# Kernel optimization log

Hardware: AMD Instinct MI355X
Metric: run time of the kernel (lower is better)

The kernel has to match this reference:

```python
import jax, jax.numpy as jnp
import numpy as np
from jax import lax

EPS = 1e-5  # BatchNorm eps (eval mode, running stats)
HEADS = 8

# --- surrogate-gradient Heaviside (sigmoid surrogate, alpha=4) ---
@jax.custom_vjp
def spike(u):
    return (u >= 0.0).astype(u.dtype)

def _spike_fwd(u):
    return spike(u), u

def _spike_bwd(u, g):
    s = jax.nn.sigmoid(4.0 * u)
    return (g * 4.0 * s * (1.0 - s),)

spike.defvjp(_spike_fwd, _spike_bwd)

def lif(x, tau=0.5, threshold=1.0):
    """Multi-step LIF over leading time axis: v_t = tau*v_{t-1} + x_t,
    s_t = H(v_t - threshold), hard reset v_t *= (1 - s_t)."""
    def step(v, xt):
        v = tau * v + xt
        s = spike(v - threshold)
        return v * (1.0 - s), s
    _, out = lax.scan(step, jnp.zeros_like(x[0]), x)
    return out

def bn_eval(x, gamma, beta, mean, var):
    # x: (T,B,C,N); per-channel affine using running stats
    inv = gamma / jnp.sqrt(var + EPS)
    return x * inv[None, None, :, None] + (beta - mean * inv)[None, None, :, None]

def setup_inputs() -> dict:
    key = jax.random.key(0)
    ks = jax.random.split(key, 12)
    T, B, C, H, W = 4, 32, 384, 16, 16
    d = {}
    d['x'] = jax.random.normal(ks[0], (T, B, C, H, W), dtype=jnp.float32)
    # 1x1 Conv1d weights == (C_out, C_in) matrices
    sc = 1.0 / np.sqrt(C)
    d['q_w'] = jax.random.normal(ks[1], (C, C), dtype=jnp.float32) * sc
    d['q_gamma'] = jnp.ones((C,), jnp.float32)
    d['q_beta'] = jnp.zeros((C,), jnp.float32)
    d['q_mean'] = jax.random.normal(ks[2], (C,), dtype=jnp.float32) * 0.1
    d['q_var'] = jax.random.uniform(ks[3], (C,), dtype=jnp.float32) + 0.5
    d['k_w'] = jax.random.normal(ks[4], (C, C), dtype=jnp.float32) * sc
    d['k_gamma'] = jnp.ones((C,), jnp.float32)
    d['k_beta'] = jnp.zeros((C,), jnp.float32)
    d['k_mean'] = jax.random.normal(ks[5], (C,), dtype=jnp.float32) * 0.1
    d['k_var'] = jax.random.uniform(ks[6], (C,), dtype=jnp.float32) + 0.5
    d['proj_w'] = jax.random.normal(ks[7], (C, C), dtype=jnp.float32) * sc
    d['proj_b'] = jax.random.normal(ks[8], (C,), dtype=jnp.float32) * 0.01
    d['proj_gamma'] = jnp.ones((C,), jnp.float32)
    d['proj_beta'] = jnp.zeros((C,), jnp.float32)
    d['proj_mean'] = jax.random.normal(ks[9], (C,), dtype=jnp.float32) * 0.1
    d['proj_var'] = jax.random.uniform(ks[10], (C,), dtype=jnp.float32) + 0.5
    d['mem_alpha'] = jnp.float32(0.2)
    return d

def reference(x, q_w, q_gamma, q_beta, q_mean, q_var,
              k_w, k_gamma, k_beta, k_mean, k_var,
              proj_w, proj_b, proj_gamma, proj_beta, proj_mean, proj_var,
              mem_alpha):
    T, B, C, H, W = x.shape
    Hh = HEADS
    Dh = C // Hh
    N = H * W
    # proj_lif applied to raw input, then flatten spatial dims
    s = lif(x, tau=0.5, threshold=1.0).reshape(T, B, C, N)
    # q path: 1x1 conv (channel GEMM) -> BN -> LIF
    q = lif(bn_eval(jnp.einsum('tbcn,dc->tbdn', s, q_w), q_gamma, q_beta, q_mean, q_var),
            tau=0.5, threshold=1.0).reshape(T, B, Hh, Dh, N)
    # k path
    k = lif(bn_eval(jnp.einsum('tbcn,dc->tbdn', s, k_w), k_gamma, k_beta, k_mean, k_var),
            tau=0.5, threshold=1.0).reshape(T, B, Hh, Dh, N)
    # temporal decayed memory: m_0 = q_0; m_t = alpha*m_{t-1} + (1-alpha)*q_{t-1}
    def mstep(m_prev, q_prev):
        m = mem_alpha * m_prev + (1.0 - mem_alpha) * q_prev
        return m, m
    _, mems_rest = lax.scan(mstep, q[0], q[:-1])
    mems = jnp.concatenate([q[:1], mems_rest], axis=0)  # (T,B,Hh,Dh,N)
    # cat along Dh then sum == sum(mems)+sum(q)
    q_sum = jnp.sum(mems, axis=3, keepdims=True) + jnp.sum(q, axis=3, keepdims=True)
    attn = lif(q_sum, tau=0.5, threshold=0.5)  # (T,B,Hh,1,N)
    y = (attn * k).reshape(T, B, C, N)
    # proj conv (with bias) -> BN -> reshape back to (T,B,C,H,W)
    y = jnp.einsum('tbcn,dc->tbdn', y, proj_w) + proj_b[None, None, :, None]
    y = bn_eval(y, proj_gamma, proj_beta, proj_mean, proj_var)
    return y.reshape(T, B, C, H, W)
```

## Files before the change

kernel.cpp:

```cpp
#include <hip/hip_runtime.h>

#define T_ 4
#define B_ 32
#define C_ 384
#define N_ 256
#define HEADS_ 8
#define DH_ 48
#define EPS_ 1e-5f
#define NW_ (C_*C_)

typedef _Float16 f16;
typedef __attribute__((ext_vector_type(8))) _Float16 f16x8;
typedef __attribute__((ext_vector_type(16))) float f32x16;

#define PSCALE     4096.0f
#define PSCALE_INV (1.0f/4096.0f)
#define SPIKE_BYTE 0x3Cu

__device__ __forceinline__ void unpack4(unsigned int w, unsigned int& lo, unsigned int& hi) {
#if defined(__has_builtin) && __has_builtin(__builtin_amdgcn_perm)
    lo = __builtin_amdgcn_perm(w, w, 0x010C000Cu);
    hi = __builtin_amdgcn_perm(w, w, 0x030C020Cu);
#else
    lo = ((w & 0xFFu) << 8) | ((w & 0xFF00u) << 16);
    hi = ((w & 0x00FF0000u) >> 8) | (w & 0xFF000000u);
#endif
}

__global__ __launch_bounds__(256)
void prep_kernel(const float* __restrict__ x, f16* __restrict__ s,
                 const float* __restrict__ qw, const float* __restrict__ kw,
                 const float* __restrict__ pw,
                 f16* __restrict__ q2, f16* __restrict__ k2, f16* __restrict__ p2)
{
    if (blockIdx.z == 32) {
        const int base = (blockIdx.y * 4 + blockIdx.x) * 256 + threadIdx.x;
        int idx = base;
#pragma unroll 4
        for (int it = 0; it < 48; ++it) {
            {
                float w = qw[idx]; f16 a = (f16)w; f16 bb = (f16)((w - (float)a) * PSCALE);
                q2[idx] = a; q2[NW_ + idx] = bb;
            }
            {
                float w = kw[idx]; f16 a = (f16)w; f16 bb = (f16)((w - (float)a) * PSCALE);
                k2[idx] = a; k2[NW_ + idx] = bb;
            }
            {
                float w = pw[idx]; f16 a = (f16)w; f16 bb = (f16)((w - (float)a) * PSCALE);
                p2[idx] = a; p2[NW_ + idx] = bb;
            }
            idx += 3072;
        }
        return;
    }

    const int tid = threadIdx.x;
    const int ng = tid & 15;
    const int cg = tid >> 4;
    const int n4 = blockIdx.x * 64 + ng * 4;
    const int c0 = blockIdx.y * 128 + cg * 8;
    const int b  = blockIdx.z;

    float v[8][4];
#pragma unroll
    for (int i = 0; i < 8; ++i)
#pragma unroll
        for (int j = 0; j < 4; ++j) v[i][j] = 0.f;

#pragma unroll
    for (int t = 0; t < T_; ++t) {
        const float* xt = x + (((size_t)t * B_ + b) * C_) * N_;
        float4 xv[8];
#pragma unroll
        for (int i = 0; i < 8; ++i)
            xv[i] = *(const float4*)&xt[(size_t)(c0 + i) * N_ + n4];
#pragma unroll
        for (int j = 0; j < 4; ++j) {
            union { f16 h[8]; uint4 q; } u;
#pragma unroll
            for (int i = 0; i < 8; ++i) {
                float xa = (j == 0) ? xv[i].x : (j == 1) ? xv[i].y
                         : (j == 2) ? xv[i].z : xv[i].w;
                float vv = 0.5f * v[i][j] + xa;
                int sp = (vv >= 1.0f) ? 1 : 0;
                v[i][j] = sp ? 0.f : vv;
                u.h[i] = sp ? (f16)1.0f : (f16)0.0f;
            }
            f16* dst = s + (((size_t)t * B_ + b) * N_ + n4 + j) * (size_t)C_ + c0;
            *(uint4*)dst = u.q;
        }
    }
}

__global__ __launch_bounds__(256)
void qk_gemm_lif_kernel(const f16* __restrict__ Wq, const f16* __restrict__ Wk,
                        const f16* __restrict__ S,
                        const float* __restrict__ qg, const float* __restrict__ qb,
                        const float* __restrict__ qm, const float* __restrict__ qv,
                        const float* __restrict__ kg, const float* __restrict__ kb,
                        const float* __restrict__ km, const float* __restrict__ kv,
                        unsigned char* __restrict__ q_spk,
                        unsigned char* __restrict__ k_spk)
{
    __shared__ __align__(16) char smem[36864];
    f16 (*As)[72]      = reinterpret_cast<f16(*)[72]>(smem);
    f16 (*Bs)[64][72]  = reinterpret_cast<f16(*)[64][72]>(smem + 18432);

    const int tid  = threadIdx.x;
    const int lane = tid & 63;
    const int wave = tid >> 6;
    const int wm = wave & 1, wd = wave >> 1;
    const int l31 = lane & 31;
    const int lhi = lane >> 5;

    const int mb = blockIdx.x;
    const int b  = mb >> 3;
    const int n0 = (mb & 7) * 32;
    const int dp0 = blockIdx.y * 64;
    const int path = (dp0 >= C_) ? 1 : 0;
    const int d0 = dp0 - path * C_;

    const f16* W = path ? Wk : Wq;
    const float* g_  = path ? kg : qg;
    const float* be_ = path ? kb : qb;
    const float* m_  = path ? km : qm;
    const float* va_ = path ? kv : qv;
    unsigned char* spk = path ? k_spk : q_spk;

    const int dcol = d0 + wd * 32 + l31;
    const float inv = g_[dcol] / sqrtf(va_[dcol] + EPS_);
    const float add = be_[dcol] - m_[dcol] * inv;

    const int ar = tid >> 1;
    const int ah = (tid & 1) * 32;
    const int at = ar >> 5;
    const int anl = ar & 31;
    const f16* arow = S + (((size_t)at * B_ + b) * N_ + n0 + anl) * (size_t)C_;
    const int aps = 4 * anl + ((at + (anl >> 1)) & 3);

    const int bp = tid >> 7;
    const int brr = (tid >> 1) & 63;
    const int bh = (tid & 1) * 32;
    const f16* brow = W + (size_t)bp * NW_ + (size_t)(d0 + brr) * C_;

    const int abase = 4 * (l31 >> 2) + ((l31 + (l31 >> 3)) & 3);
    const f16* pa0 = &As[wm * 64 + abase][0];
    const f16* pa1 = pa0 + 32 * 72;

    f32x16 acc[2][2];
#pragma unroll
    for (int ms = 0; ms < 2; ++ms)
#pragma unroll
        for (int p = 0; p < 2; ++p)
#pragma unroll
            for (int r = 0; r < 16; ++r) acc[ms][p][r] = 0.f;

    for (int kc = 0; kc < C_; kc += 64) {
        __syncthreads();
        {
            const f16* ga = arow + kc + ah;
            *(uint4*)&As[aps][ah]      = *(const uint4*)(ga);
            *(uint4*)&As[aps][ah + 8]  = *(const uint4*)(ga + 8);
            *(uint4*)&As[aps][ah + 16] = *(const uint4*)(ga + 16);
            *(uint4*)&As[aps][ah + 24] = *(const uint4*)(ga + 24);
            const f16* gb = brow + kc + bh;
            *(uint4*)&Bs[bp][brr][bh]      = *(const uint4*)(gb);
            *(uint4*)&Bs[bp][brr][bh + 8]  = *(const uint4*)(gb + 8);
            *(uint4*)&Bs[bp][brr][bh + 16] = *(const uint4*)(gb + 16);
            *(uint4*)&Bs[bp][brr][bh + 24] = *(const uint4*)(gb + 24);
        }
        __syncthreads();
#pragma unroll
        for (int kk = 0; kk < 4; ++kk) {
            const int ko = kk * 16 + lhi * 8;
            f16x8 a0 = *(const f16x8*)(pa0 + ko);
            f16x8 a1 = *(const f16x8*)(pa1 + ko);
            f16x8 b0 = *(const f16x8*)&Bs[0][wd * 32 + l31][ko];
            f16x8 b1 = *(const f16x8*)&Bs[1][wd * 32 + l31][ko];
            acc[0][0] = __builtin_amdgcn_mfma_f32_32x32x16_f16(a0, b0, acc[0][0], 0, 0, 0);
            acc[1][0] = __builtin_amdgcn_mfma_f32_32x32x16_f16(a1, b0, acc[1][0], 0, 0, 0);
            acc[0][1] = __builtin_amdgcn_mfma_f32_32x32x16_f16(a0, b1, acc[0][1], 0, 0, 0);
            acc[1][1] = __builtin_amdgcn_mfma_f32_32x32x16_f16(a1, b1, acc[1][1], 0, 0, 0);
        }
    }

#pragma unroll
    for (int ms = 0; ms < 2; ++ms)
#pragma unroll
    for (int g = 0; g < 4; ++g) {
        const int n = n0 + wm * 16 + ms * 8 + 2 * g + lhi;
        float v = 0.f;
#pragma unroll
        for (int t = 0; t < 4; ++t) {
            const int r = g * 4 + t;
            float val = (acc[ms][0][r] + acc[ms][1][r] * PSCALE_INV) * inv + add;
            float vv = 0.5f * v + val;
            int sp = (vv >= 1.0f) ? 1 : 0;
            v = sp ? 0.f : vv;
            spk[(((size_t)t * B_ + b) * N_ + n) * C_ + dcol] =
                sp ? (unsigned char)SPIKE_BYTE : (unsigned char)0;
        }
    }
}

__global__ __launch_bounds__(256)
void head_attn_kernel(const unsigned char* __restrict__ q_spk,
                      const float* __restrict__ alpha_p,
                      unsigned char* __restrict__ attn)
{
    int i = blockIdx.x * 256 + threadIdx.x;
    int n = i & (N_ - 1);
    int h = (i >> 8) & (HEADS_ - 1);
    int b = i >> 11;
    const float alpha = alpha_p[0];
    const int stride = B_ * HEADS_ * N_;
    float M = 0.f, v = 0.f, Sprev = 0.f;
#pragma unroll
    for (int t = 0; t < T_; ++t) {
        const uint4* p = (const uint4*)(q_spk + (((size_t)(t * B_ + b) * N_) + n) * C_ + h * DH_);
        int cnt = 0;
#pragma unroll
        for (int j = 0; j < 3; ++j) {
            uint4 w = p[j];
            cnt += __popc(w.x & 0x04040404u) + __popc(w.y & 0x04040404u)
                 + __popc(w.z & 0x04040404u) + __popc(w.w & 0x04040404u);
        }
        float Sqt = (float)cnt;
        if (t == 0) M = Sqt;
        else        M = alpha * M + (1.f - alpha) * Sprev;
        float qsum = M + Sqt;
        float vv = 0.5f * v + qsum;
        unsigned char sp = (vv >= 0.5f) ? 1 : 0;
        v = sp ? 0.f : vv;
        attn[(size_t)t * stride + i] = sp;
        Sprev = Sqt;
    }
}

__global__ __launch_bounds__(256)
void proj_gemm_kernel(const f16* __restrict__ Wp,
                      const unsigned char* __restrict__ K8,
                      const unsigned char* __restrict__ attn,
                      const float* __restrict__ bias,
                      const float* __restrict__ gamma, const float* __restrict__ beta,
                      const float* __restrict__ mean,  const float* __restrict__ var,
                      float* __restrict__ out)
{
    __shared__ __align__(16) char smem[36864];
    f16 (*As)[72]     = reinterpret_cast<f16(*)[72]>(smem);
    f16 (*Bs)[64][72] = reinterpret_cast<f16(*)[64][72]>(smem + 18432);

    const int tid  = threadIdx.x;
    const int lane = tid & 63;
    const int wave = tid >> 6;
    const int wm = wave & 1, wd = wave >> 1;
    const int l31 = lane & 31;
    const int lhi = lane >> 5;

    const int mb = blockIdx.x;
    const int tb = mb >> 1;
    const int n0 = (mb & 1) * 128;
    const int d0 = blockIdx.y * 64;

    const int dcol = d0 + wd * 32 + l31;
    const float iv = gamma[dcol] / sqrtf(var[dcol] + EPS_);
    const float ad = beta[dcol] - mean[dcol] * iv + bias[dcol] * iv;

    const int ar = tid >> 1;
    const int ah = (tid & 1) * 32;
    const int an = n0 + ar;
    const unsigned char* arow = K8 + ((size_t)tb * N_ + an) * (size_t)C_;
    const unsigned char* At = attn + (size_t)tb * HEADS_ * N_;

    const int bp = tid >> 7;
    const int brr = (tid >> 1) & 63;
    const int bh = (tid & 1) * 32;
    const f16* brow = Wp + (size_t)bp * NW_ + (size_t)(d0 + brr) * C_;

    f32x16 acc[2][2];
#pragma unroll
    for (int ms = 0; ms < 2; ++ms)
#pragma unroll
        for (int p = 0; p < 2; ++p)
#pragma unroll
            for (int r = 0; r < 16; ++r) acc[ms][p][r] = 0.f;

    for (int kc = 0; kc < C_; kc += 64) {
        __syncthreads();
        {
#pragma unroll
            for (int j = 0; j < 4; ++j) {
                int c = kc + ah + 8 * j;
                int h = c / DH_;
                unsigned char am = At[(size_t)h * N_ + an];
                uint2 w2 = am ? *(const uint2*)(arow + c) : make_uint2(0u, 0u);
                uint4 o;
                unpack4(w2.x, o.x, o.y);
                unpack4(w2.y, o.z, o.w);
                *(uint4*)&As[ar][ah + 8 * j] = o;
            }
            const f16* gb = brow + kc + bh;
            *(uint4*)&Bs[bp][brr][bh]      = *(const uint4*)(gb);
            *(uint4*)&Bs[bp][brr][bh + 8]  = *(const uint4*)(gb + 8);
            *(uint4*)&Bs[bp][brr][bh + 16] = *(const uint4*)(gb + 16);
            *(uint4*)&Bs[bp][brr][bh + 24] = *(const uint4*)(gb + 24);
        }
        __syncthreads();
#pragma unroll
        for (int kk = 0; kk < 4; ++kk) {
            const int ko = kk * 16 + lhi * 8;
            f16x8 a0 = *(const f16x8*)&As[wm * 64 + l31][ko];
            f16x8 a1 = *(const f16x8*)&As[wm * 64 + 32 + l31][ko];
            f16x8 b0 = *(const f16x8*)&Bs[0][wd * 32 + l31][ko];
            f16x8 b1 = *(const f16x8*)&Bs[1][wd * 32 + l31][ko];
            acc[0][0] = __builtin_amdgcn_mfma_f32_32x32x16_f16(a0, b0, acc[0][0], 0, 0, 0);
            acc[1][0] = __builtin_amdgcn_mfma_f32_32x32x16_f16(a1, b0, acc[1][0], 0, 0, 0);
            acc[0][1] = __builtin_amdgcn_mfma_f32_32x32x16_f16(a0, b1, acc[0][1], 0, 0, 0);
            acc[1][1] = __builtin_amdgcn_mfma_f32_32x32x16_f16(a1, b1, acc[1][1], 0, 0, 0);
        }
    }

    float* obase = out + ((size_t)tb * C_ + dcol) * N_;
#pragma unroll
    for (int ms = 0; ms < 2; ++ms)
#pragma unroll
    for (int r = 0; r < 16; ++r) {
        int n = n0 + wm * 64 + ms * 32 + (r & 3) + 8 * (r >> 2) + 4 * lhi;
        float val = acc[ms][0][r] + acc[ms][1][r] * PSCALE_INV;
        obase[n] = val * iv + ad;
    }
}

extern "C" void kernel_launch(void* const* d_in, const int* in_sizes, int n_in,
                              void* d_out, int out_size, void* d_ws, size_t ws_size,
                              hipStream_t stream)
{
    const float* x       = (const float*)d_in[0];
    const float* q_w     = (const float*)d_in[1];
    const float* q_gamma = (const float*)d_in[2];
    const float* q_beta  = (const float*)d_in[3];
    const float* q_mean  = (const float*)d_in[4];
    const float* q_var   = (const float*)d_in[5];
    const float* k_w     = (const float*)d_in[6];
    const float* k_gamma = (const float*)d_in[7];
    const float* k_beta  = (const float*)d_in[8];
    const float* k_mean  = (const float*)d_in[9];
    const float* k_var   = (const float*)d_in[10];
    const float* proj_w  = (const float*)d_in[11];
    const float* proj_b  = (const float*)d_in[12];
    const float* p_gamma = (const float*)d_in[13];
    const float* p_beta  = (const float*)d_in[14];
    const float* p_mean  = (const float*)d_in[15];
    const float* p_var   = (const float*)d_in[16];
    const float* m_alpha = (const float*)d_in[17];

    float* out = (float*)d_out;

    const size_t S_BYTES   = (size_t)T_ * B_ * N_ * C_ * sizeof(f16);
    const size_t SPK_BYTES = (size_t)T_ * B_ * N_ * C_;
    const size_t W2_BYTES  = (size_t)2 * NW_ * sizeof(f16);
    const size_t TBHN      = (size_t)T_ * B_ * HEADS_ * N_;

    unsigned char* ws = (unsigned char*)d_ws;
    size_t off = 0;
    auto carve = [&](size_t bytes) {
        off = (off + 255) & ~(size_t)255;
        void* p = ws + off;
        off += bytes;
        return p;
    };
    f16* s_f16  = (f16*)carve(S_BYTES);
    unsigned char* q_spk = (unsigned char*)carve(SPK_BYTES);
    unsigned char* k_spk = (unsigned char*)carve(SPK_BYTES);
    f16* Wq2    = (f16*)carve(W2_BYTES);
    f16* Wk2    = (f16*)carve(W2_BYTES);
    f16* Wp2    = (f16*)carve(W2_BYTES);
    unsigned char* attn = (unsigned char*)carve(TBHN);

    dim3 pgrid1(4, 3, 33);
    prep_kernel<<<pgrid1, 256, 0, stream>>>(x, s_f16, q_w, k_w, proj_w,
                                            Wq2, Wk2, Wp2);

    dim3 qkgrid(256, 12);
    qk_gemm_lif_kernel<<<qkgrid, 256, 0, stream>>>(Wq2, Wk2, s_f16,
                                                   q_gamma, q_beta, q_mean, q_var,
                                                   k_gamma, k_beta, k_mean, k_var,
                                                   q_spk, k_spk);

    head_attn_kernel<<<(B_ * HEADS_ * N_) / 256, 256, 0, stream>>>(q_spk, m_alpha, attn);

    dim3 pjgrid(256, 6);
    proj_gemm_kernel<<<pjgrid, 256, 0, stream>>>(Wp2, k_spk, attn, proj_b,
                                                 p_gamma, p_beta, p_mean, p_var, out);
}
```

Baseline: 225.0 us.

## Store input spikes as bytes and register-prefetch next K tile in GEMMs

The first-layer spike tensor is now written as one byte per element instead of fp16 and expanded to fp16 with byte permutes when staged into shared memory, halving that intermediate's write and read traffic. Both GEMM kernels also load the next K chunk's global data into registers right after the second barrier, so those loads overlap the MFMA loop. The proj kernel now loads its A data unconditionally instead of skipping the load when attention is zero, which adds some reads but removes branching. Register pressure goes up in exchange.

```diff
diff --git a/kernel.cpp b/kernel.cpp
--- a/kernel.cpp
+++ b/kernel.cpp
@@ -27,8 +27,13 @@
 #endif
 }
 
+__device__ __forceinline__ void unpack16(uint4 w, uint4& o0, uint4& o1) {
+    unpack4(w.x, o0.x, o0.y); unpack4(w.y, o0.z, o0.w);
+    unpack4(w.z, o1.x, o1.y); unpack4(w.w, o1.z, o1.w);
+}
+
 __global__ __launch_bounds__(256)
-void prep_kernel(const float* __restrict__ x, f16* __restrict__ s,
+void prep_kernel(const float* __restrict__ x, unsigned char* __restrict__ s,
                  const float* __restrict__ qw, const float* __restrict__ kw,
                  const float* __restrict__ pw,
                  f16* __restrict__ q2, f16* __restrict__ k2, f16* __restrict__ p2)
@@ -77,7 +82,7 @@
             xv[i] = *(const float4*)&xt[(size_t)(c0 + i) * N_ + n4];
 #pragma unroll
         for (int j = 0; j < 4; ++j) {
-            union { f16 h[8]; uint4 q; } u;
+            union { unsigned char bb[8]; uint2 u; } u;
 #pragma unroll
             for (int i = 0; i < 8; ++i) {
                 float xa = (j == 0) ? xv[i].x : (j == 1) ? xv[i].y
@@ -85,17 +90,17 @@
                 float vv = 0.5f * v[i][j] + xa;
                 int sp = (vv >= 1.0f) ? 1 : 0;
                 v[i][j] = sp ? 0.f : vv;
-                u.h[i] = sp ? (f16)1.0f : (f16)0.0f;
+                u.bb[i] = sp ? (unsigned char)SPIKE_BYTE : (unsigned char)0;
             }
-            f16* dst = s + (((size_t)t * B_ + b) * N_ + n4 + j) * (size_t)C_ + c0;
-            *(uint4*)dst = u.q;
+            unsigned char* dst = s + (((size_t)t * B_ + b) * N_ + n4 + j) * (size_t)C_ + c0;
+            *(uint2*)dst = u.u;
         }
     }
 }
 
 __global__ __launch_bounds__(256)
 void qk_gemm_lif_kernel(const f16* __restrict__ Wq, const f16* __restrict__ Wk,
-                        const f16* __restrict__ S,
+                        const unsigned char* __restrict__ S,
                         const float* __restrict__ qg, const float* __restrict__ qb,
                         const float* __restrict__ qm, const float* __restrict__ qv,
                         const float* __restrict__ kg, const float* __restrict__ kb,
@@ -136,7 +141,7 @@
     const int ah = (tid & 1) * 32;
     const int at = ar >> 5;
     const int anl = ar & 31;
-    const f16* arow = S + (((size_t)at * B_ + b) * N_ + n0 + anl) * (size_t)C_;
+    const unsigned char* arow = S + (((size_t)at * B_ + b) * N_ + n0 + anl) * (size_t)C_;
     const int aps = 4 * anl + ((at + (anl >> 1)) & 3);
 
     const int bp = tid >> 7;
@@ -156,21 +161,39 @@
 #pragma unroll
             for (int r = 0; r < 16; ++r) acc[ms][p][r] = 0.f;
 
-    for (int kc = 0; kc < C_; kc += 64) {
+    uint4 ra0 = *(const uint4*)(arow + ah);
+    uint4 ra1 = *(const uint4*)(arow + ah + 16);
+    uint4 rb0 = *(const uint4*)(brow + bh);
+    uint4 rb1 = *(const uint4*)(brow + bh + 8);
+    uint4 rb2 = *(const uint4*)(brow + bh + 16);
+    uint4 rb3 = *(const uint4*)(brow + bh + 24);
+
+#pragma unroll
+    for (int ic = 0; ic < 6; ++ic) {
         __syncthreads();
         {
-            const f16* ga = arow + kc + ah;
-            *(uint4*)&As[aps][ah]      = *(const uint4*)(ga);
-            *(uint4*)&As[aps][ah + 8]  = *(const uint4*)(ga + 8);
-            *(uint4*)&As[aps][ah + 16] = *(const uint4*)(ga + 16);
-            *(uint4*)&As[aps][ah + 24] = *(const uint4*)(ga + 24);
-            const f16* gb = brow + kc + bh;
-            *(uint4*)&Bs[bp][brr][bh]      = *(const uint4*)(gb);
-            *(uint4*)&Bs[bp][brr][bh + 8]  = *(const uint4*)(gb + 8);
-            *(uint4*)&Bs[bp][brr][bh + 16] = *(const uint4*)(gb + 16);
-            *(uint4*)&Bs[bp][brr][bh + 24] = *(const uint4*)(gb + 24);
+            uint4 o0, o1;
+            unpack16(ra0, o0, o1);
+            *(uint4*)&As[aps][ah]      = o0;
+            *(uint4*)&As[aps][ah + 8]  = o1;
+            unpack16(ra1, o0, o1);
+            *(uint4*)&As[aps][ah + 16] = o0;
+            *(uint4*)&As[aps][ah + 24] = o1;
+            *(uint4*)&Bs[bp][brr][bh]      = rb0;
+            *(uint4*)&Bs[bp][brr][bh + 8]  = rb1;
+            *(uint4*)&Bs[bp][brr][bh + 16] = rb2;
+            *(uint4*)&Bs[bp][brr][bh + 24] = rb3;
         }
         __syncthreads();
+        if (ic < 5) {
+            const int kn = ic * 64 + 64;
+            ra0 = *(const uint4*)(arow + kn + ah);
+            ra1 = *(const uint4*)(arow + kn + ah + 16);
+            rb0 = *(const uint4*)(brow + kn + bh);
+            rb1 = *(const uint4*)(brow + kn + bh + 8);
+            rb2 = *(const uint4*)(brow + kn + bh + 16);
+            rb3 = *(const uint4*)(brow + kn + bh + 24);
+        }
 #pragma unroll
         for (int kk = 0; kk < 4; ++kk) {
             const int ko = kk * 16 + lhi * 8;
@@ -286,27 +309,57 @@
 #pragma unroll
             for (int r = 0; r < 16; ++r) acc[ms][p][r] = 0.f;
 
-    for (int kc = 0; kc < C_; kc += 64) {
+    uint2 wa0, wa1, wa2, wa3;
+    unsigned char am0, am1, am2, am3;
+    uint4 rb0, rb1, rb2, rb3;
+    {
+        const int c0 = ah;
+        am0 = At[(size_t)((c0     ) / DH_) * N_ + an]; wa0 = *(const uint2*)(arow + c0);
+        am1 = At[(size_t)((c0 +  8) / DH_) * N_ + an]; wa1 = *(const uint2*)(arow + c0 + 8);
+        am2 = At[(size_t)((c0 + 16) / DH_) * N_ + an]; wa2 = *(const uint2*)(arow + c0 + 16);
+        am3 = At[(size_t)((c0 + 24) / DH_) * N_ + an]; wa3 = *(const uint2*)(arow + c0 + 24);
+        rb0 = *(const uint4*)(brow + bh);
+        rb1 = *(const uint4*)(brow + bh + 8);
+        rb2 = *(const uint4*)(brow + bh + 16);
+        rb3 = *(const uint4*)(brow + bh + 24);
+    }
+
+#pragma unroll
+    for (int ic = 0; ic < 6; ++ic) {
         __syncthreads();
         {
-#pragma unroll
-            for (int j = 0; j < 4; ++j) {
-                int c = kc + ah + 8 * j;
-                int h = c / DH_;
-                unsigned char am = At[(size_t)h * N_ + an];
-                uint2 w2 = am ? *(const uint2*)(arow + c) : make_uint2(0u, 0u);
-                uint4 o;
-                unpack4(w2.x, o.x, o.y);
-                unpack4(w2.y, o.z, o.w);
-                *(uint4*)&As[ar][ah + 8 * j] = o;
-            }
-            const f16* gb = brow + kc + bh;
-            *(uint4*)&Bs[bp][brr][bh]      = *(const uint4*)(gb);
-            *(uint4*)&Bs[bp][brr][bh + 8]  = *(const uint4*)(gb + 8);
-            *(uint4*)&Bs[bp][brr][bh + 16] = *(const uint4*)(gb + 16);
-            *(uint4*)&Bs[bp][brr][bh + 24] = *(const uint4*)(gb + 24);
+            uint2 w;
+            uint4 o;
+            w = am0 ? wa0 : make_uint2(0u, 0u);
+            unpack4(w.x, o.x, o.y); unpack4(w.y, o.z, o.w);
+            *(uint4*)&As[ar][ah] = o;
+            w = am1 ? wa1 : make_uint2(0u, 0u);
+            unpack4(w.x, o.x, o.y); unpack4(w.y, o.z, o.w);
+            *(uint4*)&As[ar][ah + 8] = o;
+            w = am2 ? wa2 : make_uint2(0u, 0u);
+            unpack4(w.x, o.x, o.y); unpack4(w.y, o.z, o.w);
+            *(uint4*)&As[ar][ah + 16] = o;
+            w = am3 ? wa3 : make_uint2(0u, 0u);
+            unpack4(w.x, o.x, o.y); unpack4(w.y, o.z, o.w);
+            *(uint4*)&As[ar][ah + 24] = o;
+            *(uint4*)&Bs[bp][brr][bh]      = rb0;
+            *(uint4*)&Bs[bp][brr][bh + 8]  = rb1;
+            *(uint4*)&Bs[bp][brr][bh + 16] = rb2;
+            *(uint4*)&Bs[bp][brr][bh + 24] = rb3;
         }
         __syncthreads();
+        if (ic < 5) {
+            const int kn = ic * 64 + 64;
+            const int c0 = kn + ah;
+            am0 = At[(size_t)((c0     ) / DH_) * N_ + an]; wa0 = *(const uint2*)(arow + c0);
+            am1 = At[(size_t)((c0 +  8) / DH_) * N_ + an]; wa1 = *(const uint2*)(arow + c0 + 8);
+            am2 = At[(size_t)((c0 + 16) / DH_) * N_ + an]; wa2 = *(const uint2*)(arow + c0 + 16);
+            am3 = At[(size_t)((c0 + 24) / DH_) * N_ + an]; wa3 = *(const uint2*)(arow + c0 + 24);
+            rb0 = *(const uint4*)(brow + kn + bh);
+            rb1 = *(const uint4*)(brow + kn + bh + 8);
+            rb2 = *(const uint4*)(brow + kn + bh + 16);
+            rb3 = *(const uint4*)(brow + kn + bh + 24);
+        }
 #pragma unroll
         for (int kk = 0; kk < 4; ++kk) {
             const int ko = kk * 16 + lhi * 8;
@@ -357,7 +410,6 @@
 
     float* out = (float*)d_out;
 
-    const size_t S_BYTES   = (size_t)T_ * B_ * N_ * C_ * sizeof(f16);
     const size_t SPK_BYTES = (size_t)T_ * B_ * N_ * C_;
     const size_t W2_BYTES  = (size_t)2 * NW_ * sizeof(f16);
     const size_t TBHN      = (size_t)T_ * B_ * HEADS_ * N_;
@@ -370,7 +422,7 @@
         off += bytes;
         return p;
     };
-    f16* s_f16  = (f16*)carve(S_BYTES);
+    unsigned char* s_u8  = (unsigned char*)carve(SPK_BYTES);
     unsigned char* q_spk = (unsigned char*)carve(SPK_BYTES);
     unsigned char* k_spk = (unsigned char*)carve(SPK_BYTES);
     f16* Wq2    = (f16*)carve(W2_BYTES);
@@ -379,11 +431,11 @@
     unsigned char* attn = (unsigned char*)carve(TBHN);
 
     dim3 pgrid1(4, 3, 33);
-    prep_kernel<<<pgrid1, 256, 0, stream>>>(x, s_f16, q_w, k_w, proj_w,
+    prep_kernel<<<pgrid1, 256, 0, stream>>>(x, s_u8, q_w, k_w, proj_w,
                                             Wq2, Wk2, Wp2);
 
     dim3 qkgrid(256, 12);
-    qk_gemm_lif_kernel<<<qkgrid, 256, 0, stream>>>(Wq2, Wk2, s_f16,
+    qk_gemm_lif_kernel<<<qkgrid, 256, 0, stream>>>(Wq2, Wk2, s_u8,
                                                    q_gamma, q_beta, q_mean, q_var,
                                                    k_gamma, k_beta, k_mean, k_var,
                                                    q_spk, k_spk);
```

After: 212.6 us. 5.5% less time.
